# Performance work log

Measured on AMD Instinct MI355X. Metric: run time of the kernel, lower is better.

Reference implementation:

```python
import jax, jax.numpy as jnp
import numpy as np

DIMS = (8, 8, 16, 16)   # 4D lattice, prod = 16384 sites
ND = len(DIMS)
N_IN = 4
N_OUT = 4
NC = 3
KERNEL_SIZE = 2
DILATION = 0
INIT_W = 1.0

W_IN = 2 * N_IN + 1                                  # 9
T_W = 2 * (N_IN * (KERNEL_SIZE - 1) * ND) + 1        # 33


def cconj(w):
    # swap matrix indices (axes 3,4) and negate imaginary part (last axis)
    wT = jnp.swapaxes(w, 3, 4)
    return wT * jnp.array([1.0, -1.0], dtype=w.dtype)


def complex_einsum(pattern, a, b, conj_a=1, conj_b=1):
    aR, aI = a[..., 0], conj_a * a[..., 1]
    bR, bI = b[..., 0], conj_b * b[..., 1]
    cR = jnp.einsum(pattern, aR, bR) - jnp.einsum(pattern, aI, bI)
    cI = jnp.einsum(pattern, aR, bI) + jnp.einsum(pattern, aI, bR)
    return jnp.stack((cR, cI), axis=-1)


def shift(a, axis, orientation):
    # dim 1 is flattened lattice; unflatten, roll along lattice axis, re-flatten
    o_s = a.shape
    n_s = (o_s[0],) + DIMS + o_s[2:]
    return jnp.roll(a.reshape(n_s), orientation, axis=axis + 1).reshape(o_s)


def transport(u, w, axis):
    # positive-orientation gauge transport: U w(x+mu) U^dagger
    ws = shift(w, axis, -1)
    ua = u[:, :, axis]                                 # [b, x, nc, nc, 2]
    wt = complex_einsum('bxij,bxwjk->bxwik', ua, ws)
    wt = complex_einsum('bxwij,bxkj->bxwik', wt, ua, conj_b=-1)
    return wt


def setup_inputs() -> dict:
    key = jax.random.key(0)
    k1, k2 = jax.random.split(key)
    n_sites = int(np.prod(DIMS))
    x = jax.random.normal(k1, (1, n_sites, ND + N_IN, NC, NC, 2), dtype=jnp.float32)
    std = INIT_W * np.sqrt(1.0 / (W_IN * T_W))
    weight = jax.random.normal(k2, (N_OUT, W_IN, T_W), dtype=jnp.float32) * std
    return {"x": x, "weight": weight}


def reference(x, weight):
    u, w = x[:, :, :ND], x[:, :, ND:]
    transported = []
    for axis in range(ND):
        wt = w
        for d in range(1, KERNEL_SIZE):
            for _ in range(DILATION + 1):
                wt = transport(u, wt, axis)
            transported.append(wt)
    t_w = jnp.concatenate(transported, axis=2)          # [b, x, n_in*(K-1)*ND, nc, nc, 2]

    w_full = jnp.concatenate([w, cconj(w)], axis=2)
    t_w_full = jnp.concatenate([t_w, cconj(t_w)], axis=2)

    # unit element channel
    unit = jnp.stack((jnp.eye(NC, dtype=x.dtype), jnp.zeros((NC, NC), dtype=x.dtype)), axis=-1)
    b, n_sites = x.shape[0], x.shape[1]
    unit_t = jnp.broadcast_to(unit[None, None, None], (b, n_sites, 1, NC, NC, 2))
    w_full = jnp.concatenate([w_full, unit_t], axis=2)       # [b, x, 9, nc, nc, 2]
    t_w_full = jnp.concatenate([t_w_full, unit_t], axis=2)   # [b, x, 33, nc, nc, 2]

    # bilinear gauge-covariant products, then weight contraction
    ww = complex_einsum('bxvij,bxwjk->bxvwik', w_full, t_w_full)  # [b, x, 9, 33, nc, nc, 2]
    w_out = jnp.einsum('uvw,bxvwijc->bxuijc', weight, ww)         # [b, x, n_out, nc, nc, 2]

    return jnp.concatenate([u, w_out], axis=2)
```

## Files before the change

### kernel.cpp

```cpp
#include <hip/hip_runtime.h>
#include <stdint.h>


#define SPB 32
#define TPB 128
#define NSITES 16384
#define TS_SITE 292
#define TS_W 18

__device__ __forceinline__ int neigh(int s, int a){
    if (a == 3) return (s & ~15)        | ((s + 1)    & 15);
    if (a == 2) return (s & ~(15 << 4)) | ((s + 16)   & (15 << 4));
    if (a == 1) return (s & ~(7 << 8))  | ((s + 256)  & (7 << 8));
    return              (s & ~(7 << 11))| ((s + 2048) & (7 << 11));
}

__global__ __launch_bounds__(TPB, 2)
void gcm_fused(const float* __restrict__ xp,
               const float* __restrict__ wgt,
               float* __restrict__ outp)
{
    __shared__ float lt[SPB * TS_SITE];
    const float2* x2 = (const float2*)xp;
    float2* o2 = (float2*)outp;

    const int tid = threadIdx.x;
    const int sl  = tid >> 2;
    const int q   = tid & 3;
    const int s   = blockIdx.x * SPB + sl;

    float ure[9], uim[9];
    {
        const float2* up = x2 + (s * 8 + q) * 9;
        #pragma unroll
        for (int e = 0; e < 9; e++){ float2 d = up[e]; ure[e] = d.x; uim[e] = d.y; }
    }
    const int sn = neigh(s, q);
    #pragma unroll
    for (int i = 0; i < 4; i++){
        float wre[9], wim[9];
        {
            const float2* wp = x2 + (sn * 8 + 4 + i) * 9;
            #pragma unroll
            for (int e = 0; e < 9; e++){ float2 d = wp[e]; wre[e] = d.x; wim[e] = d.y; }
        }
        float t1re[9], t1im[9];
        #pragma unroll
        for (int r = 0; r < 3; r++){
            #pragma unroll
            for (int k = 0; k < 3; k++){
                float ar = 0.f, ai = 0.f;
                #pragma unroll
                for (int j = 0; j < 3; j++){
                    float a_r = ure[r*3+j], a_i = uim[r*3+j];
                    float b_r = wre[j*3+k], b_i = wim[j*3+k];
                    ar = fmaf(a_r, b_r, ar); ar = fmaf(-a_i, b_i, ar);
                    ai = fmaf(a_r, b_i, ai); ai = fmaf(a_i, b_r, ai);
                }
                t1re[r*3+k] = ar; t1im[r*3+k] = ai;
            }
        }
        float* dst = &lt[sl * TS_SITE + (q * 4 + i) * TS_W];
        #pragma unroll
        for (int r = 0; r < 3; r++){
            #pragma unroll
            for (int k = 0; k < 3; k++){
                float ar = 0.f, ai = 0.f;
                #pragma unroll
                for (int j = 0; j < 3; j++){
                    float a_r = t1re[r*3+j], a_i = t1im[r*3+j];
                    float b_r = ure[k*3+j], b_i = uim[k*3+j];
                    ar = fmaf(a_r, b_r, ar); ar = fmaf(a_i, b_i, ar);
                    ai = fmaf(a_i, b_r, ai); ai = fmaf(-a_r, b_i, ai);
                }
                dst[(r*3+k)*2]     = ar;
                dst[(r*3+k)*2 + 1] = ai;
            }
        }
    }
    __syncthreads();

    {
        const float2* src = x2 + (s * 8 + q) * 9;
        float2* dst = o2 + (s * 8 + q) * 9;
        #pragma unroll
        for (int e = 0; e < 9; e++) dst[e] = src[e];
    }
    float wr[4][9], wi[4][9];
    #pragma unroll
    for (int v = 0; v < 4; v++){
        const float2* wp = x2 + (s * 8 + 4 + v) * 9;
        #pragma unroll
        for (int e = 0; e < 9; e++){ float2 d = wp[e]; wr[v][e] = d.x; wi[v][e] = d.y; }
    }
    float cre[9], cim[9];
    #pragma unroll
    for (int e = 0; e < 9; e++){ cre[e] = 0.f; cim[e] = 0.f; }

    const float* wq = wgt + q * 9 * 33;

    {
        float cv[9];
        #pragma unroll
        for (int v = 0; v < 9; v++) cv[v] = wq[v * 33 + 32];
        #pragma unroll
        for (int i = 0; i < 3; i++){
            #pragma unroll
            for (int j = 0; j < 3; j++){
                const int e = i*3+j, eT = j*3+i;
                float nr = (i == j) ? cv[8] : 0.f;
                float ni = 0.f;
                #pragma unroll
                for (int v = 0; v < 4; v++){
                    nr = fmaf(cv[v],    wr[v][e],  nr);
                    nr = fmaf(cv[4+v],  wr[v][eT], nr);
                    ni = fmaf(cv[v],    wi[v][e],  ni);
                    ni = fmaf(-cv[4+v], wi[v][eT], ni);
                }
                cre[e] += nr; cim[e] += ni;
            }
        }
    }

    const float* tbase = &lt[sl * TS_SITE];
    #pragma unroll 2
    for (int w16 = 0; w16 < 16; w16++){
        float tre[9], tim[9];
        {
            const float* tp = tbase + w16 * TS_W;
            #pragma unroll
            for (int e = 0; e < 9; e++){ tre[e] = tp[2*e]; tim[e] = tp[2*e+1]; }
        }
        float nre[9], nim[9];

        {
            float cv[9];
            #pragma unroll
            for (int v = 0; v < 9; v++) cv[v] = wq[v * 33 + w16];
            #pragma unroll
            for (int i = 0; i < 3; i++){
                #pragma unroll
                for (int j = 0; j < 3; j++){
                    const int e = i*3+j, eT = j*3+i;
                    float nr = (i == j) ? cv[8] : 0.f;
                    float ni = 0.f;
                    #pragma unroll
                    for (int v = 0; v < 4; v++){
                        nr = fmaf(cv[v],    wr[v][e],  nr);
                        nr = fmaf(cv[4+v],  wr[v][eT], nr);
                        ni = fmaf(cv[v],    wi[v][e],  ni);
                        ni = fmaf(-cv[4+v], wi[v][eT], ni);
                    }
                    nre[e] = nr; nim[e] = ni;
                }
            }
        }
        #pragma unroll
        for (int i = 0; i < 3; i++){
            #pragma unroll
            for (int k = 0; k < 3; k++){
                float ar = cre[i*3+k], ai = cim[i*3+k];
                #pragma unroll
                for (int j = 0; j < 3; j++){
                    float n_r = nre[i*3+j], n_i = nim[i*3+j];
                    float b_r = tre[j*3+k], b_i = tim[j*3+k];
                    ar = fmaf(n_r, b_r, ar); ar = fmaf(-n_i, b_i, ar);
                    ai = fmaf(n_r, b_i, ai); ai = fmaf(n_i, b_r, ai);
                }
                cre[i*3+k] = ar; cim[i*3+k] = ai;
            }
        }

        {
            float cv[9];
            #pragma unroll
            for (int v = 0; v < 9; v++) cv[v] = wq[v * 33 + 16 + w16];
            #pragma unroll
            for (int i = 0; i < 3; i++){
                #pragma unroll
                for (int j = 0; j < 3; j++){
                    const int e = i*3+j, eT = j*3+i;
                    float nr = (i == j) ? cv[8] : 0.f;
                    float ni = 0.f;
                    #pragma unroll
                    for (int v = 0; v < 4; v++){
                        nr = fmaf(cv[v],    wr[v][e],  nr);
                        nr = fmaf(cv[4+v],  wr[v][eT], nr);
                        ni = fmaf(cv[v],    wi[v][e],  ni);
                        ni = fmaf(-cv[4+v], wi[v][eT], ni);
                    }
                    nre[e] = nr; nim[e] = ni;
                }
            }
        }
        #pragma unroll
        for (int i = 0; i < 3; i++){
            #pragma unroll
            for (int k = 0; k < 3; k++){
                float ar = cre[i*3+k], ai = cim[i*3+k];
                #pragma unroll
                for (int j = 0; j < 3; j++){
                    float n_r = nre[i*3+j], n_i = nim[i*3+j];
                    float b_r = tre[k*3+j], b_i = tim[k*3+j];
                    ar = fmaf(n_r, b_r, ar); ar = fmaf(n_i, b_i, ar);
                    ai = fmaf(-n_r, b_i, ai); ai = fmaf(n_i, b_r, ai);
                }
                cre[i*3+k] = ar; cim[i*3+k] = ai;
            }
        }
    }

    {
        float2* dst = o2 + (s * 8 + 4 + q) * 9;
        #pragma unroll
        for (int e = 0; e < 9; e++){ float2 d; d.x = cre[e]; d.y = cim[e]; dst[e] = d; }
    }
}

extern "C" void kernel_launch(void* const* d_in, const int* in_sizes, int n_in,
                              void* d_out, int out_size, void* d_ws, size_t ws_size,
                              hipStream_t stream)
{
    const float* x = (const float*)d_in[0];
    const float* w = (const float*)d_in[1];
    float* out = (float*)d_out;
    dim3 grid(NSITES / SPB);
    dim3 block(TPB);
    hipLaunchKernelGGL(gcm_fused, grid, block, 0, stream, x, w, out);
}
```

Baseline: 90.65 us.

## Split per-site work across 16 threads with shuffle reduction and shared weights

```diff
diff --git a/kernel.cpp b/kernel.cpp
--- a/kernel.cpp
+++ b/kernel.cpp
@@ -2,11 +2,12 @@
 #include <stdint.h>
 
 
-#define SPB 32
-#define TPB 128
+#define SPB 16
+#define TPB 256
 #define NSITES 16384
 #define TS_SITE 292
 #define TS_W 18
+#define NWGT 1188
 
 __device__ __forceinline__ int neigh(int s, int a){
     if (a == 3) return (s & ~15)        | ((s + 1)    & 15);
@@ -15,35 +16,36 @@
     return              (s & ~(7 << 11))| ((s + 2048) & (7 << 11));
 }
 
-__global__ __launch_bounds__(TPB, 2)
+__global__ __launch_bounds__(TPB, 3)
 void gcm_fused(const float* __restrict__ xp,
                const float* __restrict__ wgt,
                float* __restrict__ outp)
 {
     __shared__ float lt[SPB * TS_SITE];
+    __shared__ float wsm[NWGT];
     const float2* x2 = (const float2*)xp;
     float2* o2 = (float2*)outp;
 
     const int tid = threadIdx.x;
-    const int sl  = tid >> 2;
-    const int q   = tid & 3;
+    const int g   = tid & 3;
+    const int u   = (tid >> 2) & 3;
+    const int sl  = tid >> 4;
     const int s   = blockIdx.x * SPB + sl;
 
-    float ure[9], uim[9];
+    for (int idx = tid; idx < NWGT; idx += TPB) wsm[idx] = wgt[idx];
+
     {
-        const float2* up = x2 + (s * 8 + q) * 9;
+        const int a = u, i = g;
+        float ure[9], uim[9];
+        const float2* up = x2 + (s * 8 + a) * 9;
         #pragma unroll
         for (int e = 0; e < 9; e++){ float2 d = up[e]; ure[e] = d.x; uim[e] = d.y; }
-    }
-    const int sn = neigh(s, q);
-    #pragma unroll
-    for (int i = 0; i < 4; i++){
+        const int sn = neigh(s, a);
         float wre[9], wim[9];
-        {
-            const float2* wp = x2 + (sn * 8 + 4 + i) * 9;
-            #pragma unroll
-            for (int e = 0; e < 9; e++){ float2 d = wp[e]; wre[e] = d.x; wim[e] = d.y; }
-        }
+        const float2* wp = x2 + (sn * 8 + 4 + i) * 9;
+        #pragma unroll
+        for (int e = 0; e < 9; e++){ float2 d = wp[e]; wre[e] = d.x; wim[e] = d.y; }
+
         float t1re[9], t1im[9];
         #pragma unroll
         for (int r = 0; r < 3; r++){
@@ -60,7 +62,7 @@
                 t1re[r*3+k] = ar; t1im[r*3+k] = ai;
             }
         }
-        float* dst = &lt[sl * TS_SITE + (q * 4 + i) * TS_W];
+        float* dst = &lt[sl * TS_SITE + (a * 4 + i) * TS_W];
         #pragma unroll
         for (int r = 0; r < 3; r++){
             #pragma unroll
@@ -80,12 +82,13 @@
     }
     __syncthreads();
 
-    {
-        const float2* src = x2 + (s * 8 + q) * 9;
-        float2* dst = o2 + (s * 8 + q) * 9;
+    if (g == 1){
+        const float2* src = x2 + (s * 8 + u) * 9;
+        float2* dst = o2 + (s * 8 + u) * 9;
         #pragma unroll
         for (int e = 0; e < 9; e++) dst[e] = src[e];
     }
+
     float wr[4][9], wi[4][9];
     #pragma unroll
     for (int v = 0; v < 4; v++){
@@ -93,50 +96,49 @@
         #pragma unroll
         for (int e = 0; e < 9; e++){ float2 d = wp[e]; wr[v][e] = d.x; wi[v][e] = d.y; }
     }
+
     float cre[9], cim[9];
     #pragma unroll
     for (int e = 0; e < 9; e++){ cre[e] = 0.f; cim[e] = 0.f; }
 
-    const float* wq = wgt + q * 9 * 33;
+    const float* wu = wsm + u * 297;
 
     {
-        float cv[9];
-        #pragma unroll
-        for (int v = 0; v < 9; v++) cv[v] = wq[v * 33 + 32];
+        float c1 = wu[g * 33 + 32];
+        float c2 = wu[(4 + g) * 33 + 32];
         #pragma unroll
         for (int i = 0; i < 3; i++){
             #pragma unroll
             for (int j = 0; j < 3; j++){
                 const int e = i*3+j, eT = j*3+i;
-                float nr = (i == j) ? cv[8] : 0.f;
-                float ni = 0.f;
-                #pragma unroll
-                for (int v = 0; v < 4; v++){
-                    nr = fmaf(cv[v],    wr[v][e],  nr);
-                    nr = fmaf(cv[4+v],  wr[v][eT], nr);
-                    ni = fmaf(cv[v],    wi[v][e],  ni);
-                    ni = fmaf(-cv[4+v], wi[v][eT], ni);
-                }
-                cre[e] += nr; cim[e] += ni;
-            }
+                cre[e] = fmaf(c1, wr[g][e],  cre[e]);
+                cre[e] = fmaf(c2, wr[g][eT], cre[e]);
+                cim[e] = fmaf(c1, wi[g][e],  cim[e]);
+                cim[e] = fmaf(-c2, wi[g][eT], cim[e]);
+            }
+        }
+        if (g == 0){
+            float c8 = wu[8 * 33 + 32];
+            cre[0] += c8; cre[4] += c8; cre[8] += c8;
         }
     }
 
     const float* tbase = &lt[sl * TS_SITE];
-    #pragma unroll 2
-    for (int w16 = 0; w16 < 16; w16++){
+    #pragma unroll
+    for (int k = 0; k < 4; k++){
+        const int w16 = g * 4 + k;
         float tre[9], tim[9];
         {
-            const float* tp = tbase + w16 * TS_W;
-            #pragma unroll
-            for (int e = 0; e < 9; e++){ tre[e] = tp[2*e]; tim[e] = tp[2*e+1]; }
+            const float2* tp = (const float2*)(tbase + w16 * TS_W);
+            #pragma unroll
+            for (int e = 0; e < 9; e++){ float2 d = tp[e]; tre[e] = d.x; tim[e] = d.y; }
         }
         float nre[9], nim[9];
 
         {
             float cv[9];
             #pragma unroll
-            for (int v = 0; v < 9; v++) cv[v] = wq[v * 33 + w16];
+            for (int v = 0; v < 9; v++) cv[v] = wu[v * 33 + w16];
             #pragma unroll
             for (int i = 0; i < 3; i++){
                 #pragma unroll
@@ -158,23 +160,23 @@
         #pragma unroll
         for (int i = 0; i < 3; i++){
             #pragma unroll
-            for (int k = 0; k < 3; k++){
-                float ar = cre[i*3+k], ai = cim[i*3+k];
+            for (int kk = 0; kk < 3; kk++){
+                float ar = cre[i*3+kk], ai = cim[i*3+kk];
                 #pragma unroll
                 for (int j = 0; j < 3; j++){
                     float n_r = nre[i*3+j], n_i = nim[i*3+j];
-                    float b_r = tre[j*3+k], b_i = tim[j*3+k];
+                    float b_r = tre[j*3+kk], b_i = tim[j*3+kk];
                     ar = fmaf(n_r, b_r, ar); ar = fmaf(-n_i, b_i, ar);
                     ai = fmaf(n_r, b_i, ai); ai = fmaf(n_i, b_r, ai);
                 }
-                cre[i*3+k] = ar; cim[i*3+k] = ai;
+                cre[i*3+kk] = ar; cim[i*3+kk] = ai;
             }
         }
 
         {
             float cv[9];
             #pragma unroll
-            for (int v = 0; v < 9; v++) cv[v] = wq[v * 33 + 16 + w16];
+            for (int v = 0; v < 9; v++) cv[v] = wu[v * 33 + 16 + w16];
             #pragma unroll
             for (int i = 0; i < 3; i++){
                 #pragma unroll
@@ -196,22 +198,29 @@
         #pragma unroll
         for (int i = 0; i < 3; i++){
             #pragma unroll
-            for (int k = 0; k < 3; k++){
-                float ar = cre[i*3+k], ai = cim[i*3+k];
+            for (int kk = 0; kk < 3; kk++){
+                float ar = cre[i*3+kk], ai = cim[i*3+kk];
                 #pragma unroll
                 for (int j = 0; j < 3; j++){
                     float n_r = nre[i*3+j], n_i = nim[i*3+j];
-                    float b_r = tre[k*3+j], b_i = tim[k*3+j];
+                    float b_r = tre[kk*3+j], b_i = tim[kk*3+j];
                     ar = fmaf(n_r, b_r, ar); ar = fmaf(n_i, b_i, ar);
                     ai = fmaf(-n_r, b_i, ai); ai = fmaf(n_i, b_r, ai);
                 }
-                cre[i*3+k] = ar; cim[i*3+k] = ai;
-            }
-        }
-    }
-
-    {
-        float2* dst = o2 + (s * 8 + 4 + q) * 9;
+                cre[i*3+kk] = ar; cim[i*3+kk] = ai;
+            }
+        }
+    }
+
+    #pragma unroll
+    for (int e = 0; e < 9; e++){
+        cre[e] += __shfl_xor(cre[e], 1);
+        cre[e] += __shfl_xor(cre[e], 2);
+        cim[e] += __shfl_xor(cim[e], 1);
+        cim[e] += __shfl_xor(cim[e], 2);
+    }
+    if (g == 0){
+        float2* dst = o2 + (s * 8 + 4 + u) * 9;
         #pragma unroll
         for (int e = 0; e < 9; e++){ float2 d; d.x = cre[e]; d.y = cim[e]; dst[e] = d; }
     }
```

Result: slower. 198.8 us (+119.3%).
